# Kernel optimization log

Hardware: AMD Instinct MI355X
Metric: run time of the kernel (lower is better)

## Reference

```python
import jax, jax.numpy as jnp
import numpy as np

B, T, C, H = 2, 2048, 1024, 16
HS = C // H  # 64
EPS = 1e-5


def layer_norm(x, w, b):
    mu = jnp.mean(x, axis=-1, keepdims=True)
    var = jnp.var(x, axis=-1, keepdims=True)
    return (x - mu) * jax.lax.rsqrt(var + EPS) * w + b


def setup_inputs() -> dict:
    key = jax.random.key(0)
    ks = jax.random.split(key, 16)
    s_c = 1.0 / np.sqrt(C)
    s_f = 1.0 / np.sqrt(4 * C)
    u = lambda k, shape, s: jax.random.uniform(k, shape, jnp.float32, -s, s)
    return {
        "x": jax.random.normal(ks[0], (B, T, C), jnp.float32),
        # per-head Q/K/V Linears stacked over heads: [H, C, HS], bias [H, HS]
        "Wq": u(ks[1], (H, C, HS), s_c), "bq": u(ks[2], (H, HS), s_c),
        "Wk": u(ks[3], (H, C, HS), s_c), "bk": u(ks[4], (H, HS), s_c),
        "Wv": u(ks[5], (H, C, HS), s_c), "bv": u(ks[6], (H, HS), s_c),
        "Wp": u(ks[7], (C, C), s_c), "bp": u(ks[8], (C,), s_c),
        "W1": u(ks[9], (C, 4 * C), s_c), "b1": u(ks[10], (4 * C,), s_c),
        "W2": u(ks[11], (4 * C, C), s_f), "b2": u(ks[12], (C,), s_f),
        "ln1_w": jnp.ones((C,), jnp.float32), "ln1_b": jnp.zeros((C,), jnp.float32),
        "ln2_w": jnp.ones((C,), jnp.float32), "ln2_b": jnp.zeros((C,), jnp.float32),
    }


def reference(x, Wq, bq, Wk, bk, Wv, bv, Wp, bp, W1, b1, W2, b2,
              ln1_w, ln1_b, ln2_w, ln2_b):
    # --- pre-norm self-attention ---
    xn = layer_norm(x, ln1_w, ln1_b)
    q = jnp.einsum('btc,hcd->bhtd', xn, Wq) + bq[None, :, None, :]
    k = jnp.einsum('btc,hcd->bhtd', xn, Wk) + bk[None, :, None, :]
    v = jnp.einsum('btc,hcd->bhtd', xn, Wv) + bv[None, :, None, :]
    # NOTE: original scales by C**-0.5 (full embedding dim), not head_size**-0.5
    att = jnp.einsum('bhtd,bhsd->bhts', q, k) * (C ** -0.5)
    att = jax.nn.softmax(att, axis=-1)
    o = jnp.einsum('bhts,bhsd->bhtd', att, v)  # [B,H,T,HS]
    o = jnp.transpose(o, (0, 2, 1, 3)).reshape(B, T, C)  # concat heads
    sa = o @ Wp + bp
    out = x + sa
    # --- pre-norm FFN (exact erf GELU, matching nn.GELU default) ---
    on = layer_norm(out, ln2_w, ln2_b)
    h = jax.nn.gelu(on @ W1 + b1, approximate=False)
    return out + (h @ W2 + b2)
```

## Files before the change

### kernel.cpp

```cpp
#include <hip/hip_runtime.h>
#include <math.h>

#define BB 2
#define TT 2048
#define CC 1024
#define HH 16
#define HS 64
#define MT 4096
#define FF 4096

typedef unsigned short u16;
typedef __bf16 bfrag __attribute__((ext_vector_type(8)));
typedef float f4 __attribute__((ext_vector_type(4)));

#define AS1(p) ((const __attribute__((address_space(1))) void*)(p))
#define AS3(p) ((__attribute__((address_space(3))) void*)(p))

__device__ __forceinline__ u16 f2bf(float f) {
  union { float f; unsigned u; } a; a.f = f;
  return (u16)((a.u + 0x7fffu + ((a.u >> 16) & 1u)) >> 16);
}
__device__ __forceinline__ float bf2f(u16 u) {
  union { unsigned u; float f; } a; a.u = ((unsigned)u) << 16; return a.f;
}

__device__ __forceinline__ int swz128(int byteoff) {
  return byteoff ^ (((byteoff >> 7) & 7) << 4);
}
__device__ __forceinline__ int swzAB(int byteoff) {
  return byteoff ^ (((byteoff >> 7) & 3) << 4);
}

#define XCD_SWZ_2D(BX, BY)                                                     \
  int _fl = (int)blockIdx.y * gridDim.x + blockIdx.x;                          \
  const int _nw = gridDim.x * gridDim.y;                                       \
  _fl = (_fl & 7) * (_nw >> 3) + (_fl >> 3);                                   \
  const int BX = _fl % gridDim.x;                                              \
  const int BY = _fl / gridDim.x;

__global__ void tr_f32_bf16(const float* __restrict__ src, u16* __restrict__ dst,
                            int R, int Cc, long long sb, long long db, int dld) {
  __shared__ float t[32][33];
  const int bz = blockIdx.z;
  const int r0 = blockIdx.y * 32, c0 = blockIdx.x * 32;
  const int tx = threadIdx.x, ty = threadIdx.y;
  const float* s = src + bz * sb;
  u16* d = dst + bz * db;
#pragma unroll
  for (int i = 0; i < 4; i++)
    t[ty + i * 8][tx] = s[(size_t)(r0 + ty + i * 8) * Cc + c0 + tx];
  __syncthreads();
#pragma unroll
  for (int i = 0; i < 4; i++)
    d[(size_t)(c0 + ty + i * 8) * dld + r0 + tx] = f2bf(t[tx][ty + i * 8]);
}

__global__ void tr_bf16(const u16* __restrict__ src, u16* __restrict__ dst,
                        int R, int Cc, long long sb, long long db, int dld) {
  __shared__ u16 t[32][33];
  const int bz = blockIdx.z;
  const int r0 = blockIdx.y * 32, c0 = blockIdx.x * 32;
  const int tx = threadIdx.x, ty = threadIdx.y;
  const u16* s = src + bz * sb;
  u16* d = dst + bz * db;
#pragma unroll
  for (int i = 0; i < 4; i++)
    t[ty + i * 8][tx] = s[(size_t)(r0 + ty + i * 8) * Cc + c0 + tx];
  __syncthreads();
#pragma unroll
  for (int i = 0; i < 4; i++)
    d[(size_t)(c0 + ty + i * 8) * dld + r0 + tx] = t[tx][ty + i * 8];
}

__global__ __launch_bounds__(256) void ln_kernel(
    const float* __restrict__ x, const float* __restrict__ w,
    const float* __restrict__ b, u16* __restrict__ y) {
  const int row = blockIdx.x, tid = threadIdx.x;
  const float4 v = reinterpret_cast<const float4*>(x + (size_t)row * CC)[tid];
  float s = v.x + v.y + v.z + v.w;
  float s2 = v.x * v.x + v.y * v.y + v.z * v.z + v.w * v.w;
#pragma unroll
  for (int off = 32; off >= 1; off >>= 1) {
    s += __shfl_xor(s, off);
    s2 += __shfl_xor(s2, off);
  }
  __shared__ float ps[4], ps2[4];
  const int wave = tid >> 6, lane = tid & 63;
  if (lane == 0) { ps[wave] = s; ps2[wave] = s2; }
  __syncthreads();
  s = ps[0] + ps[1] + ps[2] + ps[3];
  s2 = ps2[0] + ps2[1] + ps2[2] + ps2[3];
  const float mu = s * (1.f / CC);
  const float rstd = rsqrtf(s2 * (1.f / CC) - mu * mu + 1e-5f);
  const float4 wv = reinterpret_cast<const float4*>(w)[tid];
  const float4 bv = reinterpret_cast<const float4*>(b)[tid];
  ushort4 o;
  o.x = f2bf((v.x - mu) * rstd * wv.x + bv.x);
  o.y = f2bf((v.y - mu) * rstd * wv.y + bv.y);
  o.z = f2bf((v.z - mu) * rstd * wv.z + bv.z);
  o.w = f2bf((v.w - mu) * rstd * wv.w + bv.w);
  reinterpret_cast<ushort4*>(y + (size_t)row * CC)[tid] = o;
}

template<int NJ>
__device__ __forceinline__ void gemm_core(
    u16* smem, const u16* __restrict__ A, const u16* __restrict__ Bt,
    int K, int lda, int ldb, int bmi, int bni, f4 (&acc)[4][NJ]) {
  constexpr int BN = NJ * 32;
  constexpr int BBUF = BN * 32;
  u16* As = smem;
  u16* Bs = smem + 3 * 4096;
  const int tid = threadIdx.x;
  const int wave = tid >> 6, lane = tid & 63;
  const int wm = wave >> 1, wn = wave & 1;
  const int lg = lane >> 4, ll = lane & 15;

  const int trow = tid >> 2;
  const int tch  = (tid & 3) ^ ((trow >> 1) & 3);
  const u16* ga = A + (size_t)(bmi * 128 + trow) * lda + tch * 8;
  const u16* gb = Bt + (size_t)(bni * BN + trow) * ldb + tch * 8;
  const size_t g64a = (size_t)64 * lda;
  const size_t g64b = (size_t)64 * ldb;
  const int nt = K >> 5;

  auto GSTAGE = [&](int bi, int kt) {
    u16* la = &As[bi * 4096 + tid * 8];
    u16* lb = &Bs[bi * BBUF + tid * 8];
    const u16* gA = ga + kt * 32;
    const u16* gB = gb + kt * 32;
    __builtin_amdgcn_global_load_lds(AS1(gA), AS3(la), 16, 0, 0);
    __builtin_amdgcn_global_load_lds(AS1(gA + g64a), AS3(la + 2048), 16, 0, 0);
    __builtin_amdgcn_global_load_lds(AS1(gB), AS3(lb), 16, 0, 0);
    if constexpr (NJ == 4)
      __builtin_amdgcn_global_load_lds(AS1(gB + g64b), AS3(lb + 2048), 16, 0, 0);
  };

  GSTAGE(0, 0);
  GSTAGE(1, 1);
  GSTAGE(2, 2);
  int bi = 0;
  for (int t = 0; t < nt; t++) {
    const int ahead = nt - 1 - t;
    if constexpr (NJ == 4) {
      if (ahead >= 2)      asm volatile("s_waitcnt vmcnt(8)" ::: "memory");
      else if (ahead == 1) asm volatile("s_waitcnt vmcnt(4)" ::: "memory");
      else                 asm volatile("s_waitcnt vmcnt(0)" ::: "memory");
    } else {
      if (ahead >= 2)      asm volatile("s_waitcnt vmcnt(6)" ::: "memory");
      else if (ahead == 1) asm volatile("s_waitcnt vmcnt(3)" ::: "memory");
      else                 asm volatile("s_waitcnt vmcnt(0)" ::: "memory");
    }
    __builtin_amdgcn_s_barrier();
    __builtin_amdgcn_sched_barrier(0);

    const char* as_ = (const char*)(As + bi * 4096);
    const char* bs_ = (const char*)(Bs + bi * BBUF);
    bfrag af[4], bf[NJ];
#pragma unroll
    for (int i = 0; i < 4; i++)
      af[i] = *(const bfrag*)(as_ + swzAB((wm * 64 + i * 16 + ll) * 64 + lg * 16));
#pragma unroll
    for (int j = 0; j < NJ; j++)
      bf[j] = *(const bfrag*)(bs_ + swzAB((wn * (BN / 2) + j * 16 + ll) * 64 + lg * 16));

    __builtin_amdgcn_s_setprio(1);
#pragma unroll
    for (int i = 0; i < 4; i++)
#pragma unroll
      for (int j = 0; j < NJ; j++)
        acc[i][j] = __builtin_amdgcn_mfma_f32_16x16x32_bf16(af[i], bf[j], acc[i][j], 0, 0, 0);
    __builtin_amdgcn_s_setprio(0);

    __builtin_amdgcn_sched_barrier(0);
    __builtin_amdgcn_s_barrier();
    if (t + 3 < nt) GSTAGE(bi, t + 3);
    bi = (bi == 2) ? 0 : bi + 1;
  }
}

#define EPI_COORDS                                              \
  const int tid = threadIdx.x;                                  \
  const int wave = tid >> 6, lane = tid & 63;                   \
  const int wm = wave >> 1, wn = wave & 1;                      \
  const int lg = lane >> 4, ll = lane & 15;

__global__ __launch_bounds__(256, 3) void gemm_qkv(
    const u16* __restrict__ A, const u16* __restrict__ Bt,
    const float* __restrict__ bq, const float* __restrict__ bk,
    const float* __restrict__ bv,
    u16* __restrict__ q, u16* __restrict__ k, u16* __restrict__ v) {
  __shared__ u16 smem[24576];
  XCD_SWZ_2D(bx, by)
  f4 acc[4][4] = {};
  gemm_core<4>(smem, A, Bt, CC, CC, CC, by, bx, acc);
  EPI_COORDS
  __syncthreads();
#pragma unroll
  for (int j = 0; j < 4; j++) {
    const int n = bx * 128 + wn * 64 + j * 16 + ll;
    const int sec = n >> 10, nn = n & 1023;
    const float bias = (sec == 0 ? bq : (sec == 1 ? bk : bv))[nn];
    const float scale = (sec == 0) ? 0.045084220027780106f : 1.0f;
#pragma unroll
    for (int i = 0; i < 4; i++)
#pragma unroll
      for (int r = 0; r < 4; r++)
        smem[(wm * 64 + i * 16 + lg * 4 + r) * 136 + wn * 64 + j * 16 + ll] =
            f2bf((acc[i][j][r] + bias) * scale);
  }
  __syncthreads();
  const int rr = tid >> 4, cb = (tid & 15) * 8;
#pragma unroll
  for (int R = 0; R < 8; R++) {
    const int row = R * 16 + rr;
    const int m = by * 128 + row, b = m >> 11, t = m & 2047;
    const int n = bx * 128 + cb;
    const int sec = n >> 10, nn = n & 1023, h = nn >> 6, d = nn & 63;
    u16* dst = sec == 0 ? q : (sec == 1 ? k : v);
    *(uint4*)&dst[(((size_t)b * HH + h) * TT + t) * HS + d] =
        *(const uint4*)&smem[row * 136 + cb];
  }
}

__global__ __launch_bounds__(256, 3) void gemm_ffn1(
    const u16* __restrict__ A, const u16* __restrict__ Bt,
    const float* __restrict__ b1, u16* __restrict__ hb) {
  __shared__ u16 smem[24576];
  XCD_SWZ_2D(bx, by)
  f4 acc[4][4] = {};
  gemm_core<4>(smem, A, Bt, CC, CC, CC, by, bx, acc);
  EPI_COORDS
  __syncthreads();
#pragma unroll
  for (int j = 0; j < 4; j++) {
    const int n = bx * 128 + wn * 64 + j * 16 + ll;
    const float bias = b1[n];
#pragma unroll
    for (int i = 0; i < 4; i++)
#pragma unroll
      for (int r = 0; r < 4; r++) {
        const float t = acc[i][j][r] + bias;
        const float g = 0.5f * t * (1.0f + erff(t * 0.70710678118654752f));
        smem[(wm * 64 + i * 16 + lg * 4 + r) * 136 + wn * 64 + j * 16 + ll] = f2bf(g);
      }
  }
  __syncthreads();
  const int rr = tid >> 4, cb = (tid & 15) * 8;
#pragma unroll
  for (int R = 0; R < 8; R++) {
    const int row = R * 16 + rr;
    *(uint4*)&hb[(size_t)(by * 128 + row) * FF + bx * 128 + cb] =
        *(const uint4*)&smem[row * 136 + cb];
  }
}

__global__ __launch_bounds__(256, 3) void gemm_ffn2sk(
    const u16* __restrict__ A, const u16* __restrict__ Bt,
    u16* __restrict__ p0, u16* __restrict__ p1) {
  __shared__ u16 smem[24576];
  int _fl = ((int)blockIdx.z * gridDim.y + blockIdx.y) * gridDim.x + blockIdx.x;
  const int _nw = gridDim.x * gridDim.y * gridDim.z;
  _fl = (_fl & 7) * (_nw >> 3) + (_fl >> 3);
  const int bx = _fl % gridDim.x;
  const int by = (_fl / gridDim.x) % gridDim.y;
  const int bz = _fl / (gridDim.x * gridDim.y);

  f4 acc[4][4] = {};
  gemm_core<4>(smem, A + bz * 2048, Bt + bz * 2048, 2048, FF, FF, by, bx, acc);
  EPI_COORDS
  __syncthreads();
#pragma unroll
  for (int j = 0; j < 4; j++)
#pragma unroll
    for (int i = 0; i < 4; i++)
#pragma unroll
      for (int r = 0; r < 4; r++)
        smem[(wm * 64 + i * 16 + lg * 4 + r) * 136 + wn * 64 + j * 16 + ll] =
            f2bf(acc[i][j][r]);
  __syncthreads();
  u16* pp = bz ? p1 : p0;
  const int rr = tid >> 4, cb = (tid & 15) * 8;
#pragma unroll
  for (int R = 0; R < 8; R++) {
    const int row = R * 16 + rr;
    *(uint4*)&pp[(size_t)(by * 128 + row) * CC + bx * 128 + cb] =
        *(const uint4*)&smem[row * 136 + cb];
  }
}

__global__ __launch_bounds__(256) void ffn2_reduce(
    const u16* __restrict__ p0, const u16* __restrict__ p1,
    const float* __restrict__ b2, float* __restrict__ dout) {
  const int gid = blockIdx.x * 256 + threadIdx.x;
  const int n0 = (gid * 8) & (CC - 1);
  const uint4 a = ((const uint4*)p0)[gid];
  const uint4 c = ((const uint4*)p1)[gid];
  const u16* au = (const u16*)&a;
  const u16* cu = (const u16*)&c;
  float4 d0 = ((const float4*)dout)[gid * 2];
  float4 d1 = ((const float4*)dout)[gid * 2 + 1];
  const float4 w0 = *(const float4*)&b2[n0];
  const float4 w1 = *(const float4*)&b2[n0 + 4];
  d0.x += w0.x + bf2f(au[0]) + bf2f(cu[0]);
  d0.y += w0.y + bf2f(au[1]) + bf2f(cu[1]);
  d0.z += w0.z + bf2f(au[2]) + bf2f(cu[2]);
  d0.w += w0.w + bf2f(au[3]) + bf2f(cu[3]);
  d1.x += w1.x + bf2f(au[4]) + bf2f(cu[4]);
  d1.y += w1.y + bf2f(au[5]) + bf2f(cu[5]);
  d1.z += w1.z + bf2f(au[6]) + bf2f(cu[6]);
  d1.w += w1.w + bf2f(au[7]) + bf2f(cu[7]);
  ((float4*)dout)[gid * 2] = d0;
  ((float4*)dout)[gid * 2 + 1] = d1;
}

__global__ __launch_bounds__(256, 3) void gemm_proj(
    const u16* __restrict__ A, const u16* __restrict__ Bt,
    const float* __restrict__ bp, const float* __restrict__ x,
    float* __restrict__ outw) {
  __shared__ u16 smem[18432];
  XCD_SWZ_2D(bx, by)
  f4 acc[4][2] = {};
  gemm_core<2>(smem, A, Bt, CC, CC, CC, by, bx, acc);
  EPI_COORDS
#pragma unroll
  for (int i = 0; i < 4; i++)
#pragma unroll
    for (int j = 0; j < 2; j++) {
      const int n = bx * 64 + wn * 32 + j * 16 + ll;
      const float bias = bp[n];
#pragma unroll
      for (int r = 0; r < 4; r++) {
        const int m = by * 128 + wm * 64 + i * 16 + lg * 4 + r;
        const size_t idx = (size_t)m * CC + n;
        outw[idx] = acc[i][j][r] + bias + x[idx];
      }
    }
}

__global__ __launch_bounds__(256, 4) void attn_kernel(
    const u16* __restrict__ Q, const u16* __restrict__ Kb,
    const u16* __restrict__ Vt, u16* __restrict__ Ao) {
  __shared__ __align__(1024) u16 Ks[2][64 * 64];
  __shared__ __align__(1024) u16 Vs[2][64 * 64];
  __shared__ __align__(1024) u16 Ps[4][16 * 64];
  const int bh = blockIdx.y, qt = blockIdx.x;
  const int tid = threadIdx.x, wave = tid >> 6, lane = tid & 63;
  const int lg = lane >> 4, ll = lane & 15;

  bfrag qf[2];
  const u16* Qb = Q + ((size_t)bh * TT + qt * 64 + wave * 16) * HS;
#pragma unroll
  for (int dc = 0; dc < 2; dc++)
    qf[dc] = *(const bfrag*)&Qb[ll * HS + dc * 32 + lg * 8];

  f4 o[4] = {};
  float mrun = -INFINITY, lrun = 0.f;

  const int trow = tid >> 3;
  const int tch  = (tid & 7) ^ (trow & 7);
  const u16* gk = Kb + ((size_t)bh * TT + trow) * HS + tch * 8;
  const u16* gv = Vt + ((size_t)bh * HS + trow) * TT + tch * 8;

  char* const pw = (char*)Ps[wave];

#define STAGE(bufi, stt)                                                          \
  do {                                                                            \
    u16* lk = &Ks[bufi][tid * 8];                                                 \
    u16* lv = &Vs[bufi][tid * 8];                                                 \
    __builtin_amdgcn_global_load_lds(AS1(gk + (size_t)(stt) * HS), AS3(lk), 16, 0, 0); \
    __builtin_amdgcn_global_load_lds(AS1(gk + (size_t)(stt) * HS + 32 * HS), AS3(lk + 2048), 16, 0, 0); \
    __builtin_amdgcn_global_load_lds(AS1(gv + (stt)), AS3(lv), 16, 0, 0);         \
    __builtin_amdgcn_global_load_lds(AS1(gv + (stt) + (size_t)32 * TT), AS3(lv + 2048), 16, 0, 0); \
  } while (0)

  STAGE(0, 0);
  int cur = 0;

  for (int st = 0; st < TT; st += 64) {
    if (st + 64 < TT) {
      STAGE(cur ^ 1, st + 64);
      asm volatile("s_waitcnt vmcnt(4)" ::: "memory");
    } else {
      asm volatile("s_waitcnt vmcnt(0)" ::: "memory");
    }
    __builtin_amdgcn_s_barrier();
    __builtin_amdgcn_sched_barrier(0);

    const char* kbuf = (const char*)Ks[cur];
    const char* vbuf = (const char*)Vs[cur];

    f4 p[4];
#pragma unroll
    for (int kb = 0; kb < 4; kb++) {
      const int row = kb * 16 + ll;
      const bfrag k0 = *(const bfrag*)(kbuf + swz128(row * 128 + lg * 16));
      const bfrag k1 = *(const bfrag*)(kbuf + swz128(row * 128 + 64 + lg * 16));
      f4 z = {0.f, 0.f, 0.f, 0.f};
      z = __builtin_amdgcn_mfma_f32_16x16x32_bf16(k0, qf[0], z, 0, 0, 0);
      p[kb] = __builtin_amdgcn_mfma_f32_16x16x32_bf16(k1, qf[1], z, 0, 0, 0);
    }

    {
      float pm = p[0][0];
#pragma unroll
      for (int kb = 0; kb < 4; kb++)
#pragma unroll
        for (int r = 0; r < 4; r++)
          if (kb | r) pm = fmaxf(pm, p[kb][r]);
      pm = fmaxf(pm, __shfl_xor(pm, 16));
      pm = fmaxf(pm, __shfl_xor(pm, 32));
      const float mn = fmaxf(mrun, pm);
      const float al = exp2f(mrun - mn);
      mrun = mn;
      float rs = 0.f;
#pragma unroll
      for (int kb = 0; kb < 4; kb++)
#pragma unroll
        for (int r = 0; r < 4; r++) {
          const float e = exp2f(p[kb][r] - mn);
          p[kb][r] = e;
          rs += e;
        }
      rs += __shfl_xor(rs, 16);
      rs += __shfl_xor(rs, 32);
      lrun = lrun * al + rs;
#pragma unroll
      for (int fo = 0; fo < 4; fo++) o[fo] *= al;
#pragma unroll
      for (int kb = 0; kb < 4; kb++) {
        union { uint2 v; __bf16 h[4]; } w;
        w.h[0] = (__bf16)p[kb][0];
        w.h[1] = (__bf16)p[kb][1];
        w.h[2] = (__bf16)p[kb][2];
        w.h[3] = (__bf16)p[kb][3];
        *(uint2*)(pw + swz128(ll * 128 + kb * 32 + lg * 8)) = w.v;
      }
    }

#pragma unroll
    for (int ks = 0; ks < 2; ks++) {
      const bfrag pb = *(const bfrag*)(pw + swz128(ll * 128 + ks * 64 + lg * 16));
#pragma unroll
      for (int fo = 0; fo < 4; fo++) {
        const bfrag vf = *(const bfrag*)(vbuf + swz128((fo * 16 + ll) * 128 + ks * 64 + lg * 16));
        o[fo] = __builtin_amdgcn_mfma_f32_16x16x32_bf16(vf, pb, o[fo], 0, 0, 0);
      }
    }

    __builtin_amdgcn_sched_barrier(0);
    __builtin_amdgcn_s_barrier();
    cur ^= 1;
  }
#undef STAGE

  const int b = bh >> 4, h = bh & 15;
  const float inv = 1.0f / lrun;
  const int t = qt * 64 + wave * 16 + ll;
#pragma unroll
  for (int fo = 0; fo < 4; fo++) {
    union { uint2 v; __bf16 hh[4]; } w;
    w.hh[0] = (__bf16)(o[fo][0] * inv);
    w.hh[1] = (__bf16)(o[fo][1] * inv);
    w.hh[2] = (__bf16)(o[fo][2] * inv);
    w.hh[3] = (__bf16)(o[fo][3] * inv);
    *(uint2*)&Ao[((size_t)b * TT + t) * CC + h * HS + fo * 16 + lg * 4] = w.v;
  }
}

extern "C" void kernel_launch(void* const* d_in, const int* in_sizes, int n_in,
                              void* d_out, int out_size, void* d_ws, size_t ws_size,
                              hipStream_t stream) {
  const float* x    = (const float*)d_in[0];
  const float* Wq   = (const float*)d_in[1];
  const float* bq   = (const float*)d_in[2];
  const float* Wk   = (const float*)d_in[3];
  const float* bk   = (const float*)d_in[4];
  const float* Wv   = (const float*)d_in[5];
  const float* bv   = (const float*)d_in[6];
  const float* Wp   = (const float*)d_in[7];
  const float* bp   = (const float*)d_in[8];
  const float* W1   = (const float*)d_in[9];
  const float* b1   = (const float*)d_in[10];
  const float* W2   = (const float*)d_in[11];
  const float* b2   = (const float*)d_in[12];
  const float* ln1w = (const float*)d_in[13];
  const float* ln1b = (const float*)d_in[14];
  const float* ln2w = (const float*)d_in[15];
  const float* ln2b = (const float*)d_in[16];
  float* dout = (float*)d_out;

  char* ws = (char*)d_ws;
  u16* wqkv = (u16*)(ws + 0);
  u16* wpt  = (u16*)(ws + 6291456);
  u16* w1t  = (u16*)(ws + 8388608);
  u16* w2t  = (u16*)(ws + 16777216);
  u16* xn   = (u16*)(ws + 25165824);
  u16* qb   = (u16*)(ws + 33554432);
  u16* kb   = (u16*)(ws + 41943040);
  u16* vb   = (u16*)(ws + 50331648);
  u16* vt   = (u16*)(ws + 58720256);
  u16* ao   = (u16*)(ws + 67108864);
  u16* hb   = qb;
  u16* pk0  = (u16*)(ws + 0);
  u16* pk1  = (u16*)(ws + 8388608);

  dim3 blk256(256);
  dim3 blkT(32, 8);

  tr_f32_bf16<<<dim3(2, 32, 16), blkT, 0, stream>>>(Wq, wqkv,               1024,   64, 65536LL, 65536LL, 1024);
  tr_f32_bf16<<<dim3(2, 32, 16), blkT, 0, stream>>>(Wk, wqkv + 1024 * 1024, 1024,   64, 65536LL, 65536LL, 1024);
  tr_f32_bf16<<<dim3(2, 32, 16), blkT, 0, stream>>>(Wv, wqkv + 2048 * 1024, 1024,   64, 65536LL, 65536LL, 1024);
  tr_f32_bf16<<<dim3(32, 32, 1),  blkT, 0, stream>>>(Wp, wpt, 1024, 1024, 0LL, 0LL, 1024);
  tr_f32_bf16<<<dim3(128, 32, 1), blkT, 0, stream>>>(W1, w1t, 1024, 4096, 0LL, 0LL, 1024);
  tr_f32_bf16<<<dim3(32, 128, 1), blkT, 0, stream>>>(W2, w2t, 4096, 1024, 0LL, 0LL, 4096);

  ln_kernel<<<dim3(MT), blk256, 0, stream>>>(x, ln1w, ln1b, xn);

  gemm_qkv<<<dim3(24, 32), blk256, 0, stream>>>(xn, wqkv, bq, bk, bv, qb, kb, vb);

  tr_bf16<<<dim3(2, 64, 32), blkT, 0, stream>>>(vb, vt, 2048, 64, 131072LL, 131072LL, 2048);

  attn_kernel<<<dim3(32, 32), blk256, 0, stream>>>(qb, kb, vt, ao);

  gemm_proj<<<dim3(16, 32), blk256, 0, stream>>>(ao, wpt, bp, x, dout);

  ln_kernel<<<dim3(MT), blk256, 0, stream>>>(dout, ln2w, ln2b, xn);

  gemm_ffn1<<<dim3(32, 32), blk256, 0, stream>>>(xn, w1t, b1, hb);
  gemm_ffn2sk<<<dim3(8, 32, 2), blk256, 0, stream>>>(hb, w2t, pk0, pk1);
  ffn2_reduce<<<dim3(MT * CC / 8 / 256), blk256, 0, stream>>>(pk0, pk1, b2, dout);
}
```

Baseline: 277.5 us.

## Remap attention block order, hoist swizzle offsets, skip unneeded online-softmax rescale

Remaps the flat block index so consecutive blocks share the same few batch-heads, which should improve L2 reuse of K/V. Precomputes the swizzled LDS offsets once, outside the key loop. Reorganizes the max and sum reductions as trees to shorten dependency chains. Skips the accumulator rescale when no lane's row max increased, using a wave-wide vote; this adds a branch in exchange for skipping exp and multiply work.

```diff
diff --git a/kernel.cpp b/kernel.cpp
--- a/kernel.cpp
+++ b/kernel.cpp
@@ -343,7 +343,12 @@
   __shared__ __align__(1024) u16 Ks[2][64 * 64];
   __shared__ __align__(1024) u16 Vs[2][64 * 64];
   __shared__ __align__(1024) u16 Ps[4][16 * 64];
-  const int bh = blockIdx.y, qt = blockIdx.x;
+
+  const int fl = (int)blockIdx.y * 32 + blockIdx.x;
+  const int idx = fl >> 3;
+  const int bh = (idx >> 5) * 8 + (fl & 7);
+  const int qt = idx & 31;
+
   const int tid = threadIdx.x, wave = tid >> 6, lane = tid & 63;
   const int lg = lane >> 4, ll = lane & 15;
 
@@ -362,6 +367,22 @@
   const u16* gv = Vt + ((size_t)bh * HS + trow) * TT + tch * 8;
 
   char* const pw = (char*)Ps[wave];
+
+  int koff0[4], koff1[4], pwoff[4], proff[2], voff[2][4];
+#pragma unroll
+  for (int kb = 0; kb < 4; kb++) {
+    const int row = kb * 16 + ll;
+    koff0[kb] = swz128(row * 128 + lg * 16);
+    koff1[kb] = swz128(row * 128 + 64 + lg * 16);
+    pwoff[kb] = swz128(ll * 128 + kb * 32 + lg * 8);
+  }
+#pragma unroll
+  for (int ks = 0; ks < 2; ks++) {
+    proff[ks] = swz128(ll * 128 + ks * 64 + lg * 16);
+#pragma unroll
+    for (int fo = 0; fo < 4; fo++)
+      voff[ks][fo] = swz128((fo * 16 + ll) * 128 + ks * 64 + lg * 16);
+  }
 
 #define STAGE(bufi, stt)                                                          \
   do {                                                                            \
@@ -392,40 +413,50 @@
     f4 p[4];
 #pragma unroll
     for (int kb = 0; kb < 4; kb++) {
-      const int row = kb * 16 + ll;
-      const bfrag k0 = *(const bfrag*)(kbuf + swz128(row * 128 + lg * 16));
-      const bfrag k1 = *(const bfrag*)(kbuf + swz128(row * 128 + 64 + lg * 16));
+      const bfrag k0 = *(const bfrag*)(kbuf + koff0[kb]);
+      const bfrag k1 = *(const bfrag*)(kbuf + koff1[kb]);
       f4 z = {0.f, 0.f, 0.f, 0.f};
       z = __builtin_amdgcn_mfma_f32_16x16x32_bf16(k0, qf[0], z, 0, 0, 0);
       p[kb] = __builtin_amdgcn_mfma_f32_16x16x32_bf16(k1, qf[1], z, 0, 0, 0);
     }
 
     {
-      float pm = p[0][0];
-#pragma unroll
-      for (int kb = 0; kb < 4; kb++)
-#pragma unroll
-        for (int r = 0; r < 4; r++)
-          if (kb | r) pm = fmaxf(pm, p[kb][r]);
+      f4 m01, m23;
+#pragma unroll
+      for (int r = 0; r < 4; r++) {
+        m01[r] = fmaxf(p[0][r], p[1][r]);
+        m23[r] = fmaxf(p[2][r], p[3][r]);
+      }
+#pragma unroll
+      for (int r = 0; r < 4; r++) m01[r] = fmaxf(m01[r], m23[r]);
+      float pm = fmaxf(fmaxf(m01[0], m01[1]), fmaxf(m01[2], m01[3]));
       pm = fmaxf(pm, __shfl_xor(pm, 16));
       pm = fmaxf(pm, __shfl_xor(pm, 32));
-      const float mn = fmaxf(mrun, pm);
-      const float al = exp2f(mrun - mn);
-      mrun = mn;
-      float rs = 0.f;
+      if (!__all((int)(pm <= mrun))) {
+        const float mn = fmaxf(mrun, pm);
+        const float al = exp2f(mrun - mn);
+        mrun = mn;
+        lrun *= al;
+#pragma unroll
+        for (int fo = 0; fo < 4; fo++) o[fo] *= al;
+      }
 #pragma unroll
       for (int kb = 0; kb < 4; kb++)
 #pragma unroll
-        for (int r = 0; r < 4; r++) {
-          const float e = exp2f(p[kb][r] - mn);
-          p[kb][r] = e;
-          rs += e;
-        }
+        for (int r = 0; r < 4; r++)
+          p[kb][r] = exp2f(p[kb][r] - mrun);
+      f4 s01, s23;
+#pragma unroll
+      for (int r = 0; r < 4; r++) {
+        s01[r] = p[0][r] + p[1][r];
+        s23[r] = p[2][r] + p[3][r];
+      }
+#pragma unroll
+      for (int r = 0; r < 4; r++) s01[r] += s23[r];
+      float rs = (s01[0] + s01[1]) + (s01[2] + s01[3]);
       rs += __shfl_xor(rs, 16);
       rs += __shfl_xor(rs, 32);
-      lrun = lrun * al + rs;
-#pragma unroll
-      for (int fo = 0; fo < 4; fo++) o[fo] *= al;
+      lrun += rs;
 #pragma unroll
       for (int kb = 0; kb < 4; kb++) {
         union { uint2 v; __bf16 h[4]; } w;
@@ -433,16 +464,16 @@
         w.h[1] = (__bf16)p[kb][1];
         w.h[2] = (__bf16)p[kb][2];
         w.h[3] = (__bf16)p[kb][3];
-        *(uint2*)(pw + swz128(ll * 128 + kb * 32 + lg * 8)) = w.v;
+        *(uint2*)(pw + pwoff[kb]) = w.v;
       }
     }
 
 #pragma unroll
     for (int ks = 0; ks < 2; ks++) {
-      const bfrag pb = *(const bfrag*)(pw + swz128(ll * 128 + ks * 64 + lg * 16));
+      const bfrag pb = *(const bfrag*)(pw + proff[ks]);
 #pragma unroll
       for (int fo = 0; fo < 4; fo++) {
-        const bfrag vf = *(const bfrag*)(vbuf + swz128((fo * 16 + ll) * 128 + ks * 64 + lg * 16));
+        const bfrag vf = *(const bfrag*)(vbuf + voff[ks][fo]);
         o[fo] = __builtin_amdgcn_mfma_f32_16x16x32_bf16(vf, pb, o[fo], 0, 0, 0);
       }
     }
```

Result: no change. 277.2 us (-0.1%).
